# Performance work log

Measured on AMD Instinct MI355X. Metric: run time of the kernel, lower is better.

## Reference

```python
import jax, jax.numpy as jnp
import numpy as np
import math

B, S, D = 2, 2048, 1024
H, DH = 16, 64          # n_heads, d_head = d_model // n_heads
WINDOW = 256            # window_size


def setup_inputs() -> dict:
    key = jax.random.key(0)
    ks = jax.random.split(key, 9)
    scale = 0.02
    return {
        "x":  jax.random.normal(ks[0], (B, S, D), dtype=jnp.float32),
        "wq": jax.random.normal(ks[1], (D, D), dtype=jnp.float32) * scale,
        "bq": jnp.zeros((D,), dtype=jnp.float32),
        "wk": jax.random.normal(ks[2], (D, D), dtype=jnp.float32) * scale,
        "bk": jnp.zeros((D,), dtype=jnp.float32),
        "wv": jax.random.normal(ks[3], (D, D), dtype=jnp.float32) * scale,
        "bv": jnp.zeros((D,), dtype=jnp.float32),
        "wo": jax.random.normal(ks[4], (D, D), dtype=jnp.float32) * scale,
        "bo": jnp.zeros((D,), dtype=jnp.float32),
    }


def reference(x, wq, bq, wk, bk, wv, bv, wo, bo):
    b, s, d = x.shape
    # QKV projections -> [b, h, s, dh]
    q = (x @ wq + bq).reshape(b, s, H, DH).transpose(0, 2, 1, 3)
    k = (x @ wk + bk).reshape(b, s, H, DH).transpose(0, 2, 1, 3)
    v = (x @ wv + bv).reshape(b, s, H, DH).transpose(0, 2, 1, 3)

    scores = jnp.einsum("bhqd,bhkd->bhqk", q, k) / math.sqrt(DH)

    # causal + local-window mask: j <= i and i - j <= window
    idx = jnp.arange(s)
    row = idx[:, None]
    col = idx[None, :]
    mask = (col <= row) & (row - col <= WINDOW)        # [s, s]
    scores = jnp.where(mask[None, None, :, :], scores, -jnp.inf)

    attn = jax.nn.softmax(scores, axis=-1)
    # torch.nan_to_num(attn, 0.0): rows always include the diagonal so no NaNs,
    # but keep faithful behavior.
    attn = jnp.nan_to_num(attn, nan=0.0)

    out = jnp.einsum("bhqk,bhkd->bhqd", attn, v)        # [b, h, s, dh]
    out = out.transpose(0, 2, 1, 3).reshape(b, s, d)
    return out @ wo + bo
```

## Files before the change

### kernel.cpp

```cpp
#include <hip/hip_runtime.h>

#define B_ 2
#define S_ 2048
#define D_ 1024
#define H_ 16
#define DH_ 64
#define WIN_ 256
#define VTS 2080

typedef __attribute__((ext_vector_type(8))) short bf16x8;
typedef __attribute__((ext_vector_type(4))) float f32x4;
typedef unsigned short u16;

#define MFMA(a, b, c) __builtin_amdgcn_mfma_f32_16x16x32_bf16((a), (b), (c), 0, 0, 0)

__device__ __forceinline__ u16 f2b(float f) {
  unsigned int u = __float_as_uint(f);
  u += 0x7fffu + ((u >> 16) & 1u);
  return (u16)(u >> 16);
}

__device__ __forceinline__ float b2f(u16 b) {
  return __uint_as_float(((unsigned int)b) << 16);
}

__device__ __forceinline__ void async_cp16(const void* g, void* l) {
  __builtin_amdgcn_global_load_lds(
      (const __attribute__((address_space(1))) void*)g,
      (__attribute__((address_space(3))) void*)l, 16, 0, 0);
}

__global__ void k_prep(const float* __restrict__ x,
                       const float* __restrict__ wq, const float* __restrict__ wk,
                       const float* __restrict__ wv, const float* __restrict__ wo,
                       u16* __restrict__ xb, u16* __restrict__ wqkvt, u16* __restrict__ wot) {
  __shared__ float tile[64][65];
  const int bx = blockIdx.x;
  const int t = threadIdx.x;
  if (bx < 4096) {
    int i = (bx * 256 + t) * 4;
    float4 v = *(const float4*)(x + i);
    ushort4 o;
    o.x = f2b(v.x); o.y = f2b(v.y); o.z = f2b(v.z); o.w = f2b(v.w);
    *(ushort4*)(xb + i) = o;
    return;
  }
  const int tb = bx - 4096;
  const int z = tb >> 8, rest = tb & 255;
  const float* W = z == 0 ? wq : z == 1 ? wk : z == 2 ? wv : wo;
  u16* T = z < 3 ? wqkvt + (size_t)z * 1024 * 1024 : wot;
  const int bn = (rest & 15) * 64;
  const int bk = (rest >> 4) * 64;
  const int r = t >> 4;
  const int c = (t & 15) * 4;
#pragma unroll
  for (int i = 0; i < 4; i++) {
    float4 v = *(const float4*)(W + (size_t)(bk + r + i * 16) * D_ + bn + c);
    tile[c + 0][r + i * 16] = v.x;
    tile[c + 1][r + i * 16] = v.y;
    tile[c + 2][r + i * 16] = v.z;
    tile[c + 3][r + i * 16] = v.w;
  }
  __syncthreads();
  const int n = t >> 2, seg = (t & 3) * 16;
  __align__(16) u16 tmp[16];
#pragma unroll
  for (int u = 0; u < 16; u++) tmp[u] = f2b(tile[n][seg + u]);
  uint4* dst = (uint4*)(T + (size_t)(bn + n) * D_ + bk + seg);
  dst[0] = ((uint4*)tmp)[0];
  dst[1] = ((uint4*)tmp)[1];
}

__device__ __forceinline__ void gemm_core128(const u16* __restrict__ Ag, const u16* __restrict__ Btg,
                                             u16* As, u16* Bs, f32x4 (&acc)[4][4],
                                             int m0, int n0) {
  const int tid = threadIdx.x;
  const int w = tid >> 6, lane = tid & 63;
  const int quad = lane >> 4, l15 = lane & 15;
  const int wm = (w & 1) * 64, wn = (w >> 1) * 64;
  const int rowa = tid >> 3;
  const int colsw = (((tid & 7) ^ (rowa & 7)) * 8);
  const u16* ap = Ag + (size_t)(m0 + rowa) * D_ + colsw;
  const u16* bp = Btg + (size_t)(n0 + rowa) * D_ + colsw;
  u16* As0 = As + w * 512;
  u16* Bs0 = Bs + w * 512;
  const int c0 = ((quad * 8) ^ ((l15 & 7) * 8));
  for (int kb = 0; kb < D_; kb += 64) {
#pragma unroll
    for (int i = 0; i < 4; i++) {
      async_cp16(ap + kb + (size_t)(i * 32) * D_, As0 + i * 2048);
      async_cp16(bp + kb + (size_t)(i * 32) * D_, Bs0 + i * 2048);
    }
    __syncthreads();
#pragma unroll
    for (int kh = 0; kh < 2; kh++) {
      const int c = c0 ^ (kh * 32);
      bf16x8 af[4], bfr[4];
#pragma unroll
      for (int i = 0; i < 4; i++) af[i] = *(const bf16x8*)&As[(wm + i * 16 + l15) * 64 + c];
#pragma unroll
      for (int j = 0; j < 4; j++) bfr[j] = *(const bf16x8*)&Bs[(wn + j * 16 + l15) * 64 + c];
#pragma unroll
      for (int i = 0; i < 4; i++)
#pragma unroll
        for (int j = 0; j < 4; j++) acc[i][j] = MFMA(af[i], bfr[j], acc[i][j]);
    }
    __syncthreads();
  }
}

__global__ __launch_bounds__(256, 3) void k_gemm_qkv(
    const u16* __restrict__ xb, const u16* __restrict__ wqkvt,
    const float* __restrict__ bq, const float* __restrict__ bk_, const float* __restrict__ bv,
    u16* __restrict__ Qg, u16* __restrict__ Kg, u16* __restrict__ Vt) {
  __shared__ __align__(16) u16 smem[17408];
  u16* As = smem;
  u16* Bs = smem + 8192;
  const int L = blockIdx.x;
  const int xcd = L & 7, slot = L >> 3;
  const int mblk = (xcd >> 1) * 8 + (slot & 7);
  const int nblk = (xcd & 1) * 12 + (slot >> 3);
  const int n0 = nblk * 128, m0 = mblk * 128;
  const int z = n0 >> 10;
  const float* bias = z == 0 ? bq : z == 1 ? bk_ : bv;
  f32x4 acc[4][4] = {};
  gemm_core128(xb, wqkvt, As, Bs, acc, m0, n0);

  const int tid = threadIdx.x;
  const int w = tid >> 6, lane = tid & 63;
  const int quad = lane >> 4, l15 = lane & 15;
  const int wm = (w & 1) * 64, wn = (w >> 1) * 64;
  const int nloc = n0 & 1023;
  float biasv[4];
#pragma unroll
  for (int j = 0; j < 4; j++) biasv[j] = bias[nloc + wn + j * 16 + l15];
  const int b_ = m0 >> 11, sb = m0 & 2047;
  const float scale = z == 0 ? 0.125f * 1.44269504f : 1.0f;
  const int row = tid >> 4, ch = tid & 15;

  if (z < 2) {
#pragma unroll
    for (int j = 0; j < 4; j++)
#pragma unroll
      for (int i = 0; i < 4; i++)
#pragma unroll
        for (int r = 0; r < 4; r++)
          smem[(wm + i * 16 + quad * 4 + r) * 136 + wn + j * 16 + l15] =
              f2b((acc[i][j][r] + biasv[j]) * scale);
    __syncthreads();
    u16* OG = z == 0 ? Qg : Kg;
#pragma unroll
    for (int it = 0; it < 8; it++) {
      int rr = row + it * 16;
      bf16x8 v = *(const bf16x8*)&smem[rr * 136 + ch * 8];
      *(bf16x8*)(OG + (size_t)(m0 + rr) * D_ + nloc + ch * 8) = v;
    }
  } else {
#pragma unroll
    for (int j = 0; j < 4; j++)
#pragma unroll
      for (int i = 0; i < 4; i++)
#pragma unroll
        for (int r = 0; r < 4; r++)
          smem[(wn + j * 16 + l15) * 136 + wm + i * 16 + quad * 4 + r] =
              f2b(acc[i][j][r] + biasv[j]);
    __syncthreads();
#pragma unroll
    for (int it = 0; it < 8; it++) {
      int nn = nloc + row + it * 16;
      int h = nn >> 6, dh = nn & 63;
      bf16x8 v = *(const bf16x8*)&smem[(row + it * 16) * 136 + ch * 8];
      *(bf16x8*)(Vt + ((size_t)(b_ * H_ + h) * DH_ + dh) * VTS + sb + ch * 8) = v;
    }
  }
}

__global__ __launch_bounds__(256, 2) void k_gemm_out(
    const u16* __restrict__ Ab, const u16* __restrict__ wot,
    const float* __restrict__ bo, float* __restrict__ out) {
  __shared__ __align__(16) u16 smem[24576];
  u16* As = smem;
  u16* Bs = smem + 8192;
  const int L = blockIdx.x;
  const int xcd = L & 7, slot = L >> 3;
  const int mblk = xcd * 8 + (slot & 7);
  const int nblk = slot >> 3;
  const int n0 = nblk * 128, m0 = mblk * 64;
  const int tid = threadIdx.x;
  const int w = tid >> 6, lane = tid & 63;
  const int quad = lane >> 4, l15 = lane & 15;
  const int wn = w * 32;
  const int rowa = tid >> 4;
  const int gg = (tid & 15) ^ rowa;
  const u16* ap = Ab + (size_t)(m0 + rowa) * D_ + gg * 8;
  const u16* bp = wot + (size_t)(n0 + rowa) * D_ + gg * 8;
  u16* As0 = As + w * 512;
  u16* Bs0 = Bs + w * 512;
  f32x4 acc[4][2] = {};
  for (int kb = 0; kb < D_; kb += 128) {
#pragma unroll
    for (int i = 0; i < 4; i++)
      async_cp16(ap + kb + (size_t)(i * 16) * D_, As0 + i * 2048);
#pragma unroll
    for (int i = 0; i < 8; i++)
      async_cp16(bp + kb + (size_t)(i * 16) * D_, Bs0 + i * 2048);
    __syncthreads();
#pragma unroll
    for (int kh = 0; kh < 4; kh++) {
      const int cs = (((quad + 4 * kh) ^ l15) * 8);
      bf16x8 af[4], bfr[2];
#pragma unroll
      for (int i = 0; i < 4; i++) af[i] = *(const bf16x8*)&As[(i * 16 + l15) * 128 + cs];
#pragma unroll
      for (int j = 0; j < 2; j++) bfr[j] = *(const bf16x8*)&Bs[(wn + j * 16 + l15) * 128 + cs];
#pragma unroll
      for (int i = 0; i < 4; i++)
#pragma unroll
        for (int j = 0; j < 2; j++) acc[i][j] = MFMA(af[i], bfr[j], acc[i][j]);
    }
    __syncthreads();
  }
  float biasv[2];
#pragma unroll
  for (int j = 0; j < 2; j++) biasv[j] = bo[n0 + wn + j * 16 + l15];
#pragma unroll
  for (int j = 0; j < 2; j++)
#pragma unroll
    for (int i = 0; i < 4; i++)
#pragma unroll
      for (int r = 0; r < 4; r++)
        smem[(i * 16 + quad * 4 + r) * 136 + wn + j * 16 + l15] = f2b(acc[i][j][r] + biasv[j]);
  __syncthreads();
  const int row = tid >> 4, ch = tid & 15;
#pragma unroll
  for (int it = 0; it < 4; it++) {
    int rr = row + it * 16;
    bf16x8 v = *(const bf16x8*)&smem[rr * 136 + ch * 8];
    float4 f0, f1;
    f0.x = b2f((u16)v[0]); f0.y = b2f((u16)v[1]); f0.z = b2f((u16)v[2]); f0.w = b2f((u16)v[3]);
    f1.x = b2f((u16)v[4]); f1.y = b2f((u16)v[5]); f1.z = b2f((u16)v[6]); f1.w = b2f((u16)v[7]);
    float* dst = out + (size_t)(m0 + rr) * D_ + n0 + ch * 8;
    *(float4*)dst = f0;
    *(float4*)(dst + 4) = f1;
  }
}

__global__ __launch_bounds__(256, 4) void k_attn(
    const u16* __restrict__ Qg, const u16* __restrict__ Kg,
    const u16* __restrict__ Vt, u16* __restrict__ Ab) {
  __shared__ __align__(16) u16 Plds[4][16 * 72];
  const int tid = threadIdx.x;
  const int w = tid >> 6, lane = tid & 63;
  const int quad = lane >> 4, l15 = lane & 15;
  const int bh = blockIdx.x;
  const int qw = blockIdx.y * 64 + w * 16;
  const int b_ = bh >> 4, h = bh & 15;

  const u16* Qbase = Qg + (size_t)(b_ * S_ + qw + l15) * D_ + h * DH_ + quad * 8;
  bf16x8 aq0 = *(const bf16x8*)Qbase;
  bf16x8 aq1 = *(const bf16x8*)(Qbase + 32);

  float lr = 0.f;
  f32x4 Oacc[4] = {};

  const u16* Kb = Kg + (size_t)b_ * S_ * D_ + h * DH_ + quad * 8;
  const u16* Vb = Vt + (size_t)bh * DH_ * VTS + (size_t)l15 * VTS + quad * 8;
  const int klo = qw >= WIN_ ? ((qw - WIN_) & ~31) : 0;
  const int q = qw + l15;
  const int srcA = l15 + ((quad & 1) ? 32 : 0);
  const int srcB = srcA + 16;

  bf16x8 k00, k01, k10, k11, v0, v1, v2, v3;
  {
    const u16* Kt0 = Kb + (size_t)(klo + l15) * D_;
    k00 = *(const bf16x8*)Kt0;
    k01 = *(const bf16x8*)(Kt0 + 32);
    k10 = *(const bf16x8*)(Kt0 + (size_t)16 * D_);
    k11 = *(const bf16x8*)(Kt0 + (size_t)16 * D_ + 32);
    const u16* Vt0 = Vb + klo;
    v0 = *(const bf16x8*)(Vt0);
    v1 = *(const bf16x8*)(Vt0 + (size_t)16 * VTS);
    v2 = *(const bf16x8*)(Vt0 + (size_t)32 * VTS);
    v3 = *(const bf16x8*)(Vt0 + (size_t)48 * VTS);
  }

  for (int k0 = klo;;) {
    const int kn = k0 + 32;
    const bool more = kn < qw + 16;
    bf16x8 nk00, nk01, nk10, nk11, nv0, nv1, nv2, nv3;
    if (more) {
      const u16* Kt0 = Kb + (size_t)(kn + l15) * D_;
      nk00 = *(const bf16x8*)Kt0;
      nk01 = *(const bf16x8*)(Kt0 + 32);
      nk10 = *(const bf16x8*)(Kt0 + (size_t)16 * D_);
      nk11 = *(const bf16x8*)(Kt0 + (size_t)16 * D_ + 32);
      const u16* Vt0 = Vb + kn;
      nv0 = *(const bf16x8*)(Vt0);
      nv1 = *(const bf16x8*)(Vt0 + (size_t)16 * VTS);
      nv2 = *(const bf16x8*)(Vt0 + (size_t)32 * VTS);
      nv3 = *(const bf16x8*)(Vt0 + (size_t)48 * VTS);
    }

    f32x4 s0 = {0.f, 0.f, 0.f, 0.f}, s1 = {0.f, 0.f, 0.f, 0.f};
    __builtin_amdgcn_s_setprio(1);
    s0 = MFMA(k00, aq0, s0);
    s0 = MFMA(k01, aq1, s0);
    s1 = MFMA(k10, aq0, s1);
    s1 = MFMA(k11, aq1, s1);
    __builtin_amdgcn_s_setprio(0);

    const bool interior = (k0 >= qw + 15 - WIN_) && (k0 + 31 <= qw);
    float e[8];
    if (interior) {
#pragma unroll
      for (int r = 0; r < 4; r++) {
        float p0 = __builtin_amdgcn_exp2f(s0[r]);
        float p1 = __builtin_amdgcn_exp2f(s1[r]);
        e[r] = p0; e[4 + r] = p1;
        lr += p0 + p1;
      }
    } else {
#pragma unroll
      for (int r = 0; r < 4; r++) {
        int key0 = k0 + quad * 4 + r;
        int key1 = key0 + 16;
        float p0 = (key0 <= q && key0 + WIN_ >= q) ? __builtin_amdgcn_exp2f(s0[r]) : 0.f;
        float p1 = (key1 <= q && key1 + WIN_ >= q) ? __builtin_amdgcn_exp2f(s1[r]) : 0.f;
        e[r] = p0; e[4 + r] = p1;
        lr += p0 + p1;
      }
    }
    unsigned int s0p01 = (unsigned)f2b(e[0]) | ((unsigned)f2b(e[1]) << 16);
    unsigned int s0p23 = (unsigned)f2b(e[2]) | ((unsigned)f2b(e[3]) << 16);
    unsigned int s1p01 = (unsigned)f2b(e[4]) | ((unsigned)f2b(e[5]) << 16);
    unsigned int s1p23 = (unsigned)f2b(e[6]) | ((unsigned)f2b(e[7]) << 16);
    unsigned int a0 = (unsigned)__shfl((int)s0p01, srcA);
    unsigned int a1 = (unsigned)__shfl((int)s0p23, srcA);
    unsigned int a2 = (unsigned)__shfl((int)s0p01, srcB);
    unsigned int a3 = (unsigned)__shfl((int)s0p23, srcB);
    unsigned int c0 = (unsigned)__shfl((int)s1p01, srcA);
    unsigned int c1 = (unsigned)__shfl((int)s1p23, srcA);
    unsigned int c2 = (unsigned)__shfl((int)s1p01, srcB);
    unsigned int c3 = (unsigned)__shfl((int)s1p23, srcB);
    union { unsigned int u[4]; bf16x8 v; } pf;
    const bool lo = quad < 2;
    pf.u[0] = lo ? a0 : c0;
    pf.u[1] = lo ? a1 : c1;
    pf.u[2] = lo ? a2 : c2;
    pf.u[3] = lo ? a3 : c3;

    __builtin_amdgcn_s_setprio(1);
    Oacc[0] = MFMA(v0, pf.v, Oacc[0]);
    Oacc[1] = MFMA(v1, pf.v, Oacc[1]);
    Oacc[2] = MFMA(v2, pf.v, Oacc[2]);
    Oacc[3] = MFMA(v3, pf.v, Oacc[3]);
    __builtin_amdgcn_s_setprio(0);

    if (!more) break;
    k00 = nk00; k01 = nk01; k10 = nk10; k11 = nk11;
    v0 = nv0; v1 = nv1; v2 = nv2; v3 = nv3;
    k0 = kn;
  }

  lr += __shfl_xor(lr, 16);
  lr += __shfl_xor(lr, 32);
  const float inv = 1.0f / lr;

  u16* P = &Plds[w][0];
#pragma unroll
  for (int j = 0; j < 4; j++)
#pragma unroll
    for (int r = 0; r < 4; r++)
      P[l15 * 72 + j * 16 + quad * 4 + r] = f2b(Oacc[j][r] * inv);
  {
    int rq = lane >> 2, cc = lane & 3;
    bf16x8 ov0 = *(const bf16x8*)&P[rq * 72 + cc * 16];
    bf16x8 ov1 = *(const bf16x8*)&P[rq * 72 + cc * 16 + 8];
    u16* dst = Ab + (size_t)(b_ * S_ + qw + rq) * D_ + h * DH_ + cc * 16;
    *(bf16x8*)dst = ov0;
    *(bf16x8*)(dst + 8) = ov1;
  }
}

extern "C" void kernel_launch(void* const* d_in, const int* in_sizes, int n_in,
                              void* d_out, int out_size, void* d_ws, size_t ws_size,
                              hipStream_t stream) {
  const float* x  = (const float*)d_in[0];
  const float* wq = (const float*)d_in[1];
  const float* bq = (const float*)d_in[2];
  const float* wk = (const float*)d_in[3];
  const float* bk = (const float*)d_in[4];
  const float* wv = (const float*)d_in[5];
  const float* bv = (const float*)d_in[6];
  const float* wo = (const float*)d_in[7];
  const float* bo = (const float*)d_in[8];

  char* ws = (char*)d_ws;
  const size_t MB = 1u << 20;
  u16* Qg    = (u16*)(ws + 0 * MB);
  u16* Kg    = (u16*)(ws + 8 * MB);
  u16* Vt    = (u16*)(ws + 16 * MB);
  u16* Ab    = (u16*)(ws + 25 * MB);
  u16* xb    = (u16*)(ws + 33 * MB);
  u16* wqkvt = (u16*)(ws + 41 * MB);
  u16* wot   = (u16*)(ws + 47 * MB);

  k_prep<<<5120, 256, 0, stream>>>(x, wq, wk, wv, wo, xb, wqkvt, wot);
  k_gemm_qkv<<<768, 256, 0, stream>>>(xb, wqkvt, bq, bk, bv, Qg, Kg, Vt);
  k_attn<<<dim3(32, 32), 256, 0, stream>>>(Qg, Kg, Vt, Ab);
  k_gemm_out<<<512, 256, 0, stream>>>(Ab, wot, bo, (float*)d_out);
}
```

Baseline: 164.3 us.

## Fuse all stages into one persistent kernel with grid-wide atomic barriers

Replaces the four separate launches (prep, QKV GEMM, attention, output GEMM) with one kernel of 768 blocks. The blocks walk through each stage and meet at spin-wait global barriers built on an atomic counter, which a small init kernel resets first. The aim is to remove launch gaps and tail drain between stages. In exchange, the barrier needs all 768 blocks resident at once (launch bounds of 3 per CU with 48KB of LDS). The shared LDS size and register limit may also reduce occupancy for the attention and out stages, and the attention work becomes unevenly split across blocks.

```diff
diff --git a/kernel.cpp b/kernel.cpp
--- a/kernel.cpp
+++ b/kernel.cpp
@@ -7,6 +7,7 @@
 #define DH_ 64
 #define WIN_ 256
 #define VTS 2080
+#define NB 768
 
 typedef __attribute__((ext_vector_type(8))) short bf16x8;
 typedef __attribute__((ext_vector_type(4))) float f32x4;
@@ -30,12 +31,23 @@
       (__attribute__((address_space(3))) void*)l, 16, 0, 0);
 }
 
-__global__ void k_prep(const float* __restrict__ x,
-                       const float* __restrict__ wq, const float* __restrict__ wk,
-                       const float* __restrict__ wv, const float* __restrict__ wo,
-                       u16* __restrict__ xb, u16* __restrict__ wqkvt, u16* __restrict__ wot) {
-  __shared__ float tile[64][65];
-  const int bx = blockIdx.x;
+__device__ __forceinline__ void gbar(unsigned* cnt, unsigned target) {
+  __syncthreads();
+  if (threadIdx.x == 0) {
+    __threadfence();
+    __hip_atomic_fetch_add(cnt, 1u, __ATOMIC_ACQ_REL, __HIP_MEMORY_SCOPE_AGENT);
+    while (__hip_atomic_load(cnt, __ATOMIC_ACQUIRE, __HIP_MEMORY_SCOPE_AGENT) < target)
+      __builtin_amdgcn_s_sleep(2);
+    __threadfence();
+  }
+  __syncthreads();
+}
+
+__device__ __forceinline__ void prep_unit(int bx, const float* __restrict__ x,
+                                          const float* __restrict__ wq, const float* __restrict__ wk,
+                                          const float* __restrict__ wv, const float* __restrict__ wo,
+                                          u16* __restrict__ xb, u16* __restrict__ wqkvt,
+                                          u16* __restrict__ wot, char* smem_raw) {
   const int t = threadIdx.x;
   if (bx < 4096) {
     int i = (bx * 256 + t) * 4;
@@ -45,6 +57,7 @@
     *(ushort4*)(xb + i) = o;
     return;
   }
+  float (*tile)[65] = (float(*)[65])smem_raw;
   const int tb = bx - 4096;
   const int z = tb >> 8, rest = tb & 255;
   const float* W = z == 0 ? wq : z == 1 ? wk : z == 2 ? wv : wo;
@@ -69,6 +82,7 @@
   uint4* dst = (uint4*)(T + (size_t)(bn + n) * D_ + bk + seg);
   dst[0] = ((uint4*)tmp)[0];
   dst[1] = ((uint4*)tmp)[1];
+  __syncthreads();
 }
 
 __device__ __forceinline__ void gemm_core128(const u16* __restrict__ Ag, const u16* __restrict__ Btg,
@@ -109,14 +123,15 @@
   }
 }
 
-__global__ __launch_bounds__(256, 3) void k_gemm_qkv(
-    const u16* __restrict__ xb, const u16* __restrict__ wqkvt,
-    const float* __restrict__ bq, const float* __restrict__ bk_, const float* __restrict__ bv,
-    u16* __restrict__ Qg, u16* __restrict__ Kg, u16* __restrict__ Vt) {
-  __shared__ __align__(16) u16 smem[17408];
+__device__ __forceinline__ void qkv_unit(int L, const u16* __restrict__ xb,
+                                         const u16* __restrict__ wqkvt,
+                                         const float* __restrict__ bq, const float* __restrict__ bk_,
+                                         const float* __restrict__ bv,
+                                         u16* __restrict__ Qg, u16* __restrict__ Kg,
+                                         u16* __restrict__ Vt, char* smem_raw) {
+  u16* smem = (u16*)smem_raw;
   u16* As = smem;
   u16* Bs = smem + 8192;
-  const int L = blockIdx.x;
   const int xcd = L & 7, slot = L >> 3;
   const int mblk = (xcd >> 1) * 8 + (slot & 7);
   const int nblk = (xcd & 1) * 12 + (slot >> 3);
@@ -175,13 +190,151 @@
   }
 }
 
-__global__ __launch_bounds__(256, 2) void k_gemm_out(
-    const u16* __restrict__ Ab, const u16* __restrict__ wot,
-    const float* __restrict__ bo, float* __restrict__ out) {
-  __shared__ __align__(16) u16 smem[24576];
+__device__ __forceinline__ void attn_unit(int u, const u16* __restrict__ Qg,
+                                          const u16* __restrict__ Kg,
+                                          const u16* __restrict__ Vt, u16* __restrict__ Ab,
+                                          char* smem_raw) {
+  u16* Plds = (u16*)smem_raw;
+  const int tid = threadIdx.x;
+  const int w = tid >> 6, lane = tid & 63;
+  const int quad = lane >> 4, l15 = lane & 15;
+  const int bh = u & 31;
+  const int qw = (u >> 5) * 64 + w * 16;
+  const int b_ = bh >> 4, h = bh & 15;
+
+  const u16* Qbase = Qg + (size_t)(b_ * S_ + qw + l15) * D_ + h * DH_ + quad * 8;
+  bf16x8 aq0 = *(const bf16x8*)Qbase;
+  bf16x8 aq1 = *(const bf16x8*)(Qbase + 32);
+
+  float lr = 0.f;
+  f32x4 Oacc[4] = {};
+
+  const u16* Kb = Kg + (size_t)b_ * S_ * D_ + h * DH_ + quad * 8;
+  const u16* Vb = Vt + (size_t)bh * DH_ * VTS + (size_t)l15 * VTS + quad * 8;
+  const int klo = qw >= WIN_ ? ((qw - WIN_) & ~31) : 0;
+  const int q = qw + l15;
+  const int srcA = l15 + ((quad & 1) ? 32 : 0);
+  const int srcB = srcA + 16;
+
+  bf16x8 k00, k01, k10, k11, v0, v1, v2, v3;
+  {
+    const u16* Kt0 = Kb + (size_t)(klo + l15) * D_;
+    k00 = *(const bf16x8*)Kt0;
+    k01 = *(const bf16x8*)(Kt0 + 32);
+    k10 = *(const bf16x8*)(Kt0 + (size_t)16 * D_);
+    k11 = *(const bf16x8*)(Kt0 + (size_t)16 * D_ + 32);
+    const u16* Vt0 = Vb + klo;
+    v0 = *(const bf16x8*)(Vt0);
+    v1 = *(const bf16x8*)(Vt0 + (size_t)16 * VTS);
+    v2 = *(const bf16x8*)(Vt0 + (size_t)32 * VTS);
+    v3 = *(const bf16x8*)(Vt0 + (size_t)48 * VTS);
+  }
+
+  for (int k0 = klo;;) {
+    const int kn = k0 + 32;
+    const bool more = kn < qw + 16;
+    bf16x8 nk00, nk01, nk10, nk11, nv0, nv1, nv2, nv3;
+    if (more) {
+      const u16* Kt0 = Kb + (size_t)(kn + l15) * D_;
+      nk00 = *(const bf16x8*)Kt0;
+      nk01 = *(const bf16x8*)(Kt0 + 32);
+      nk10 = *(const bf16x8*)(Kt0 + (size_t)16 * D_);
+      nk11 = *(const bf16x8*)(Kt0 + (size_t)16 * D_ + 32);
+      const u16* Vt0 = Vb + kn;
+      nv0 = *(const bf16x8*)(Vt0);
+      nv1 = *(const bf16x8*)(Vt0 + (size_t)16 * VTS);
+      nv2 = *(const bf16x8*)(Vt0 + (size_t)32 * VTS);
+      nv3 = *(const bf16x8*)(Vt0 + (size_t)48 * VTS);
+    }
+
+    f32x4 s0 = {0.f, 0.f, 0.f, 0.f}, s1 = {0.f, 0.f, 0.f, 0.f};
+    __builtin_amdgcn_s_setprio(1);
+    s0 = MFMA(k00, aq0, s0);
+    s0 = MFMA(k01, aq1, s0);
+    s1 = MFMA(k10, aq0, s1);
+    s1 = MFMA(k11, aq1, s1);
+    __builtin_amdgcn_s_setprio(0);
+
+    const bool interior = (k0 >= qw + 15 - WIN_) && (k0 + 31 <= qw);
+    float e[8];
+    if (interior) {
+#pragma unroll
+      for (int r = 0; r < 4; r++) {
+        float p0 = __builtin_amdgcn_exp2f(s0[r]);
+        float p1 = __builtin_amdgcn_exp2f(s1[r]);
+        e[r] = p0; e[4 + r] = p1;
+        lr += p0 + p1;
+      }
+    } else {
+#pragma unroll
+      for (int r = 0; r < 4; r++) {
+        int key0 = k0 + quad * 4 + r;
+        int key1 = key0 + 16;
+        float p0 = (key0 <= q && key0 + WIN_ >= q) ? __builtin_amdgcn_exp2f(s0[r]) : 0.f;
+        float p1 = (key1 <= q && key1 + WIN_ >= q) ? __builtin_amdgcn_exp2f(s1[r]) : 0.f;
+        e[r] = p0; e[4 + r] = p1;
+        lr += p0 + p1;
+      }
+    }
+    unsigned int s0p01 = (unsigned)f2b(e[0]) | ((unsigned)f2b(e[1]) << 16);
+    unsigned int s0p23 = (unsigned)f2b(e[2]) | ((unsigned)f2b(e[3]) << 16);
+    unsigned int s1p01 = (unsigned)f2b(e[4]) | ((unsigned)f2b(e[5]) << 16);
+    unsigned int s1p23 = (unsigned)f2b(e[6]) | ((unsigned)f2b(e[7]) << 16);
+    unsigned int a0 = (unsigned)__shfl((int)s0p01, srcA);
+    unsigned int a1 = (unsigned)__shfl((int)s0p23, srcA);
+    unsigned int a2 = (unsigned)__shfl((int)s0p01, srcB);
+    unsigned int a3 = (unsigned)__shfl((int)s0p23, srcB);
+    unsigned int c0 = (unsigned)__shfl((int)s1p01, srcA);
+    unsigned int c1 = (unsigned)__shfl((int)s1p23, srcA);
+    unsigned int c2 = (unsigned)__shfl((int)s1p01, srcB);
+    unsigned int c3 = (unsigned)__shfl((int)s1p23, srcB);
+    union { unsigned int u4[4]; bf16x8 v; } pf;
+    const bool lo = quad < 2;
+    pf.u4[0] = lo ? a0 : c0;
+    pf.u4[1] = lo ? a1 : c1;
+    pf.u4[2] = lo ? a2 : c2;
+    pf.u4[3] = lo ? a3 : c3;
+
+    __builtin_amdgcn_s_setprio(1);
+    Oacc[0] = MFMA(v0, pf.v, Oacc[0]);
+    Oacc[1] = MFMA(v1, pf.v, Oacc[1]);
+    Oacc[2] = MFMA(v2, pf.v, Oacc[2]);
+    Oacc[3] = MFMA(v3, pf.v, Oacc[3]);
+    __builtin_amdgcn_s_setprio(0);
+
+    if (!more) break;
+    k00 = nk00; k01 = nk01; k10 = nk10; k11 = nk11;
+    v0 = nv0; v1 = nv1; v2 = nv2; v3 = nv3;
+    k0 = kn;
+  }
+
+  lr += __shfl_xor(lr, 16);
+  lr += __shfl_xor(lr, 32);
+  const float inv = 1.0f / lr;
+
+  u16* P = Plds + w * 1152;
+#pragma unroll
+  for (int j = 0; j < 4; j++)
+#pragma unroll
+    for (int r = 0; r < 4; r++)
+      P[l15 * 72 + j * 16 + quad * 4 + r] = f2b(Oacc[j][r] * inv);
+  {
+    int rq = lane >> 2, cc = lane & 3;
+    bf16x8 ov0 = *(const bf16x8*)&P[rq * 72 + cc * 16];
+    bf16x8 ov1 = *(const bf16x8*)&P[rq * 72 + cc * 16 + 8];
+    u16* dst = Ab + (size_t)(b_ * S_ + qw + rq) * D_ + h * DH_ + cc * 16;
+    *(bf16x8*)dst = ov0;
+    *(bf16x8*)(dst + 8) = ov1;
+  }
+}
+
+__device__ __forceinline__ void out_unit(int L, const u16* __restrict__ Ab,
+                                         const u16* __restrict__ wot,
+                                         const float* __restrict__ bo, float* __restrict__ out,
+                                         char* smem_raw) {
+  u16* smem = (u16*)smem_raw;
   u16* As = smem;
   u16* Bs = smem + 8192;
-  const int L = blockIdx.x;
   const int xcd = L & 7, slot = L >> 3;
   const int mblk = xcd * 8 + (slot & 7);
   const int nblk = slot >> 3;
@@ -245,141 +398,32 @@
   }
 }
 
-__global__ __launch_bounds__(256, 4) void k_attn(
-    const u16* __restrict__ Qg, const u16* __restrict__ Kg,
-    const u16* __restrict__ Vt, u16* __restrict__ Ab) {
-  __shared__ __align__(16) u16 Plds[4][16 * 72];
-  const int tid = threadIdx.x;
-  const int w = tid >> 6, lane = tid & 63;
-  const int quad = lane >> 4, l15 = lane & 15;
-  const int bh = blockIdx.x;
-  const int qw = blockIdx.y * 64 + w * 16;
-  const int b_ = bh >> 4, h = bh & 15;
-
-  const u16* Qbase = Qg + (size_t)(b_ * S_ + qw + l15) * D_ + h * DH_ + quad * 8;
-  bf16x8 aq0 = *(const bf16x8*)Qbase;
-  bf16x8 aq1 = *(const bf16x8*)(Qbase + 32);
-
-  float lr = 0.f;
-  f32x4 Oacc[4] = {};
-
-  const u16* Kb = Kg + (size_t)b_ * S_ * D_ + h * DH_ + quad * 8;
-  const u16* Vb = Vt + (size_t)bh * DH_ * VTS + (size_t)l15 * VTS + quad * 8;
-  const int klo = qw >= WIN_ ? ((qw - WIN_) & ~31) : 0;
-  const int q = qw + l15;
-  const int srcA = l15 + ((quad & 1) ? 32 : 0);
-  const int srcB = srcA + 16;
-
-  bf16x8 k00, k01, k10, k11, v0, v1, v2, v3;
-  {
-    const u16* Kt0 = Kb + (size_t)(klo + l15) * D_;
-    k00 = *(const bf16x8*)Kt0;
-    k01 = *(const bf16x8*)(Kt0 + 32);
-    k10 = *(const bf16x8*)(Kt0 + (size_t)16 * D_);
-    k11 = *(const bf16x8*)(Kt0 + (size_t)16 * D_ + 32);
-    const u16* Vt0 = Vb + klo;
-    v0 = *(const bf16x8*)(Vt0);
-    v1 = *(const bf16x8*)(Vt0 + (size_t)16 * VTS);
-    v2 = *(const bf16x8*)(Vt0 + (size_t)32 * VTS);
-    v3 = *(const bf16x8*)(Vt0 + (size_t)48 * VTS);
-  }
-
-  for (int k0 = klo;;) {
-    const int kn = k0 + 32;
-    const bool more = kn < qw + 16;
-    bf16x8 nk00, nk01, nk10, nk11, nv0, nv1, nv2, nv3;
-    if (more) {
-      const u16* Kt0 = Kb + (size_t)(kn + l15) * D_;
-      nk00 = *(const bf16x8*)Kt0;
-      nk01 = *(const bf16x8*)(Kt0 + 32);
-      nk10 = *(const bf16x8*)(Kt0 + (size_t)16 * D_);
-      nk11 = *(const bf16x8*)(Kt0 + (size_t)16 * D_ + 32);
-      const u16* Vt0 = Vb + kn;
-      nv0 = *(const bf16x8*)(Vt0);
-      nv1 = *(const bf16x8*)(Vt0 + (size_t)16 * VTS);
-      nv2 = *(const bf16x8*)(Vt0 + (size_t)32 * VTS);
-      nv3 = *(const bf16x8*)(Vt0 + (size_t)48 * VTS);
-    }
-
-    f32x4 s0 = {0.f, 0.f, 0.f, 0.f}, s1 = {0.f, 0.f, 0.f, 0.f};
-    __builtin_amdgcn_s_setprio(1);
-    s0 = MFMA(k00, aq0, s0);
-    s0 = MFMA(k01, aq1, s0);
-    s1 = MFMA(k10, aq0, s1);
-    s1 = MFMA(k11, aq1, s1);
-    __builtin_amdgcn_s_setprio(0);
-
-    const bool interior = (k0 >= qw + 15 - WIN_) && (k0 + 31 <= qw);
-    float e[8];
-    if (interior) {
-#pragma unroll
-      for (int r = 0; r < 4; r++) {
-        float p0 = __builtin_amdgcn_exp2f(s0[r]);
-        float p1 = __builtin_amdgcn_exp2f(s1[r]);
-        e[r] = p0; e[4 + r] = p1;
-        lr += p0 + p1;
-      }
-    } else {
-#pragma unroll
-      for (int r = 0; r < 4; r++) {
-        int key0 = k0 + quad * 4 + r;
-        int key1 = key0 + 16;
-        float p0 = (key0 <= q && key0 + WIN_ >= q) ? __builtin_amdgcn_exp2f(s0[r]) : 0.f;
-        float p1 = (key1 <= q && key1 + WIN_ >= q) ? __builtin_amdgcn_exp2f(s1[r]) : 0.f;
-        e[r] = p0; e[4 + r] = p1;
-        lr += p0 + p1;
-      }
-    }
-    unsigned int s0p01 = (unsigned)f2b(e[0]) | ((unsigned)f2b(e[1]) << 16);
-    unsigned int s0p23 = (unsigned)f2b(e[2]) | ((unsigned)f2b(e[3]) << 16);
-    unsigned int s1p01 = (unsigned)f2b(e[4]) | ((unsigned)f2b(e[5]) << 16);
-    unsigned int s1p23 = (unsigned)f2b(e[6]) | ((unsigned)f2b(e[7]) << 16);
-    unsigned int a0 = (unsigned)__shfl((int)s0p01, srcA);
-    unsigned int a1 = (unsigned)__shfl((int)s0p23, srcA);
-    unsigned int a2 = (unsigned)__shfl((int)s0p01, srcB);
-    unsigned int a3 = (unsigned)__shfl((int)s0p23, srcB);
-    unsigned int c0 = (unsigned)__shfl((int)s1p01, srcA);
-    unsigned int c1 = (unsigned)__shfl((int)s1p23, srcA);
-    unsigned int c2 = (unsigned)__shfl((int)s1p01, srcB);
-    unsigned int c3 = (unsigned)__shfl((int)s1p23, srcB);
-    union { unsigned int u[4]; bf16x8 v; } pf;
-    const bool lo = quad < 2;
-    pf.u[0] = lo ? a0 : c0;
-    pf.u[1] = lo ? a1 : c1;
-    pf.u[2] = lo ? a2 : c2;
-    pf.u[3] = lo ? a3 : c3;
-
-    __builtin_amdgcn_s_setprio(1);
-    Oacc[0] = MFMA(v0, pf.v, Oacc[0]);
-    Oacc[1] = MFMA(v1, pf.v, Oacc[1]);
-    Oacc[2] = MFMA(v2, pf.v, Oacc[2]);
-    Oacc[3] = MFMA(v3, pf.v, Oacc[3]);
-    __builtin_amdgcn_s_setprio(0);
-
-    if (!more) break;
-    k00 = nk00; k01 = nk01; k10 = nk10; k11 = nk11;
-    v0 = nv0; v1 = nv1; v2 = nv2; v3 = nv3;
-    k0 = kn;
-  }
-
-  lr += __shfl_xor(lr, 16);
-  lr += __shfl_xor(lr, 32);
-  const float inv = 1.0f / lr;
-
-  u16* P = &Plds[w][0];
-#pragma unroll
-  for (int j = 0; j < 4; j++)
-#pragma unroll
-    for (int r = 0; r < 4; r++)
-      P[l15 * 72 + j * 16 + quad * 4 + r] = f2b(Oacc[j][r] * inv);
-  {
-    int rq = lane >> 2, cc = lane & 3;
-    bf16x8 ov0 = *(const bf16x8*)&P[rq * 72 + cc * 16];
-    bf16x8 ov1 = *(const bf16x8*)&P[rq * 72 + cc * 16 + 8];
-    u16* dst = Ab + (size_t)(b_ * S_ + qw + rq) * D_ + h * DH_ + cc * 16;
-    *(bf16x8*)dst = ov0;
-    *(bf16x8*)(dst + 8) = ov1;
-  }
+__global__ void k_init(unsigned* cnt) { *cnt = 0u; }
+
+__global__ __launch_bounds__(256, 3) void k_fused(
+    const float* __restrict__ x,
+    const float* __restrict__ wq, const float* __restrict__ wk,
+    const float* __restrict__ wv, const float* __restrict__ wo,
+    const float* __restrict__ bq, const float* __restrict__ bk_,
+    const float* __restrict__ bv, const float* __restrict__ bo,
+    u16* __restrict__ xb, u16* __restrict__ wqkvt, u16* __restrict__ wot,
+    u16* __restrict__ Qg, u16* __restrict__ Kg, u16* __restrict__ Vt,
+    u16* __restrict__ Ab, float* __restrict__ out, unsigned* cnt) {
+  __shared__ __align__(16) char smem_raw[49152];
+  const int bid = blockIdx.x;
+
+  for (int u = bid; u < 5120; u += NB)
+    prep_unit(u, x, wq, wk, wv, wo, xb, wqkvt, wot, smem_raw);
+  gbar(cnt, NB);
+
+  qkv_unit(bid, xb, wqkvt, bq, bk_, bv, Qg, Kg, Vt, smem_raw);
+  gbar(cnt, 2 * NB);
+
+  attn_unit(bid, Qg, Kg, Vt, Ab, smem_raw);
+  if (bid < 1024 - NB) attn_unit(bid + NB, Qg, Kg, Vt, Ab, smem_raw);
+  gbar(cnt, 3 * NB);
+
+  if (bid < 512) out_unit(bid, Ab, wot, bo, out, smem_raw);
 }
 
 extern "C" void kernel_launch(void* const* d_in, const int* in_sizes, int n_in,
@@ -404,9 +448,9 @@
   u16* xb    = (u16*)(ws + 33 * MB);
   u16* wqkvt = (u16*)(ws + 41 * MB);
   u16* wot   = (u16*)(ws + 47 * MB);
-
-  k_prep<<<5120, 256, 0, stream>>>(x, wq, wk, wv, wo, xb, wqkvt, wot);
-  k_gemm_qkv<<<768, 256, 0, stream>>>(xb, wqkvt, bq, bk, bv, Qg, Kg, Vt);
-  k_attn<<<dim3(32, 32), 256, 0, stream>>>(Qg, Kg, Vt, Ab);
-  k_gemm_out<<<512, 256, 0, stream>>>(Ab, wot, bo, (float*)d_out);
-}
+  unsigned* cnt = (unsigned*)(ws + 62 * MB);
+
+  k_init<<<1, 1, 0, stream>>>(cnt);
+  k_fused<<<NB, 256, 0, stream>>>(x, wq, wk, wv, wo, bq, bk, bv, bo,
+                                  xb, wqkvt, wot, Qg, Kg, Vt, Ab, (float*)d_out, cnt);
+}
```

After: 541.6 us. +229.5%, slower.
